# Kernel tuning notes

Measured on AMD Instinct MI355X. Metric: run time of the kernel, lower is better.

The kernel has to match this reference:

```python
import jax, jax.numpy as jnp
import numpy as np

NB, H, C = 6, 4, 192
B, S, L = 2, 64, 256
VOCAB, ED = 24, 64


def setup_inputs() -> dict:
    key = jax.random.key(0)
    ks = iter(jax.random.split(key, 32))
    r = lambda sh: jax.random.normal(next(ks), sh, jnp.float32) * 0.02
    z = lambda sh: jnp.zeros(sh, jnp.float32)
    return {
        'tokens': jax.random.randint(next(ks), (B, S, L), 0, VOCAB, jnp.int32),
        'emb': r((VOCAB, ED)),
        'proj_w': r((C, ED)), 'proj_b': z((C,)),
        'ln_g': jnp.ones((NB, 3, C), jnp.float32), 'ln_b': z((NB, 3, C)),
        'wq': r((NB, 2, C, C)), 'wk': r((NB, 2, C, C)),
        'wv': r((NB, 2, C, C)), 'wo': r((NB, 2, C, C)),
        'bq': z((NB, 2, C)), 'bk': z((NB, 2, C)),
        'bv': z((NB, 2, C)), 'bo': z((NB, 2, C)),
        'ffn_w1': r((NB, 4 * C, C)), 'ffn_b1': z((NB, 4 * C)),
        'ffn_w2': r((NB, C, 4 * C)), 'ffn_b2': z((NB, C)),
        'pw_w': r((C,)), 'pw_b': z(()),
    }


def rotary(x):
    # ESM-style rotary embedding over positions along dim -2, feature dim last.
    d = x.shape[-1]
    inv = 1.0 / (10000.0 ** (jnp.arange(0, d, 2, dtype=jnp.float32) / d))
    t = jnp.arange(x.shape[-2], dtype=jnp.float32)
    f = t[:, None] * inv[None, :]                  # (pos, d/2)
    emb = jnp.concatenate([f, f], axis=-1)         # (pos, d)
    cos, sin = jnp.cos(emb), jnp.sin(emb)
    x1, x2 = jnp.split(x, 2, axis=-1)
    return x * cos + jnp.concatenate([-x2, x1], axis=-1) * sin


def ln_ch(x, g, b, eps=1e-5):
    # LayerNorm over channel axis 1 of (B,C,X,Y) (== transpose->LN->transpose).
    m = x.mean(axis=1, keepdims=True)
    v = jnp.var(x, axis=1, keepdims=True)
    return (x - m) * jax.lax.rsqrt(v + eps) * g[None, :, None, None] + b[None, :, None, None]


def lin_attn(x, wq, wk, wv, wo, bq, bk, bv, bo):
    # ScaledLinearAttention: elu+1 feature map, attends over dim -2 of (B,A,N,C).
    Bm, A, N, Cm = x.shape
    dh = Cm // H
    sh = lambda t: t.reshape(Bm, A, N, H, dh).transpose(0, 1, 3, 2, 4)  # (B,A,H,N,dh)
    q = sh(x @ wq.T + bq)
    k = sh(x @ wk.T + bk)
    v = sh(x @ wv.T + bv)
    q = (jax.nn.elu(q) + 1.0) / jnp.sqrt(jnp.float32(dh))
    k = jax.nn.elu(k) + 1.0
    kv = jnp.einsum('bahnd,bahne->bahde', k, v)
    z = 1.0 / (jnp.einsum('bahnd,bahd->bahn', q, k.sum(axis=-2)) + 1e-6)
    o = jnp.einsum('bahnd,bahde->bahne', q, kv) * z[..., None]
    o = o.transpose(0, 1, 3, 2, 4).reshape(Bm, A, N, Cm)
    return o @ wo.T + bo


def fwd(tokens, emb, proj_w, proj_b, ln_g, ln_b, wq, wk, wv, wo, bq, bk, bv, bo,
        ffn_w1, ffn_b1, ffn_w2, ffn_b2, pw_w, pw_b):
    x = emb[tokens]                    # (B,S,L,ED)
    x = x @ proj_w.T + proj_b          # (B,S,L,C)
    x = rotary(x)                      # rotary over L positions
    out = jnp.transpose(x, (0, 3, 1, 2))  # (B,C,S,L)
    for i in range(NB):
        # row attention (over L)
        h = ln_ch(out, ln_g[i, 0], ln_b[i, 0])
        h = jnp.transpose(h, (0, 2, 3, 1))  # (B,S,L,C)
        h = lin_attn(h, wq[i, 0], wk[i, 0], wv[i, 0], wo[i, 0],
                     bq[i, 0], bk[i, 0], bv[i, 0], bo[i, 0])
        out = out + jnp.transpose(h, (0, 3, 1, 2))
        # col attention (over S)
        h = ln_ch(out, ln_g[i, 1], ln_b[i, 1])
        h = jnp.transpose(h, (0, 3, 2, 1))  # (B,L,S,C)
        h = lin_attn(h, wq[i, 1], wk[i, 1], wv[i, 1], wo[i, 1],
                     bq[i, 1], bk[i, 1], bv[i, 1], bo[i, 1])
        out = out + jnp.transpose(h, (0, 3, 2, 1))
        # 1x1-conv FFN
        h = ln_ch(out, ln_g[i, 2], ln_b[i, 2])
        h = jnp.einsum('bcxy,oc->boxy', h, ffn_w1[i]) + ffn_b1[i][None, :, None, None]
        h = jax.nn.gelu(h, approximate=False)
        h = jnp.einsum('bcxy,oc->boxy', h, ffn_w2[i]) + ffn_b2[i][None, :, None, None]
        out = out + h
    o = jnp.einsum('bcxy,c->bxy', out, pw_w) + pw_b   # pwFNN 1x1 conv to 1 ch
    return jax.nn.sigmoid(jax.nn.softplus(o))


def reference(tokens, emb, proj_w, proj_b, ln_g, ln_b, wq, wk, wv, wo, bq, bk, bv, bo,
              ffn_w1, ffn_b1, ffn_w2, ffn_b2, pw_w, pw_b):
    return fwd(tokens, emb, proj_w, proj_b, ln_g, ln_b, wq, wk, wv, wo, bq, bk, bv, bo,
               ffn_w1, ffn_b1, ffn_w2, ffn_b2, pw_w, pw_b)
```

## Files before the change

kernel.cpp:

```cpp
#include <hip/hip_runtime.h>
#include <hip/hip_bf16.h>
#include <math.h>

#define NBLK 6
#define NH 4
#define CCH 192
#define BB 2
#define SS 64
#define LL 256
#define DH 48
#define NP (BB*SS*LL)
#define BUF ((size_t)NP*CCH)

typedef __attribute__((ext_vector_type(8))) short short8;
typedef __attribute__((ext_vector_type(4))) float float4v;
typedef __attribute__((ext_vector_type(2))) unsigned int uintx2;

__device__ __forceinline__ unsigned short f2b(float f) {
    union { float f; unsigned int u; } v; v.f = f;
    unsigned int r = v.u + 0x7FFF + ((v.u >> 16) & 1);
    return (unsigned short)(r >> 16);
}
__device__ __forceinline__ float b2f(unsigned short u) {
    union { unsigned int u; float f; } v; v.u = ((unsigned int)u) << 16;
    return v.f;
}
__device__ __forceinline__ unsigned int cvt_pk_bf16(float lo, float hi) {
    unsigned int r;
    asm("v_cvt_pk_bf16_f32 %0, %1, %2" : "=v"(r) : "v"(lo), "v"(hi));
    return r;
}
__device__ __forceinline__ void st2u(unsigned short* p0, unsigned short* p1, float a, float b) {
    unsigned int u = cvt_pk_bf16(a, b);
    *p0 = (unsigned short)u;
    *p1 = (unsigned short)(u >> 16);
}
__device__ __forceinline__ void xf_unpack(uintx2 u, float* f) {
    union { unsigned int x; float ff; } t;
    t.x = u[0] << 16;          f[0] = t.ff;
    t.x = u[0] & 0xffff0000u;  f[1] = t.ff;
    t.x = u[1] << 16;          f[2] = t.ff;
    t.x = u[1] & 0xffff0000u;  f[3] = t.ff;
}
__device__ __forceinline__ float gelu_f(float v) {
    float z = v * 0.7071067811865475f;
    float a = fabsf(z);
    float t = __builtin_amdgcn_rcpf(fmaf(0.3275911f, a, 1.0f));
    float p = fmaf(t, 1.061405429f, -1.453152027f);
    p = fmaf(t, p, 1.421413741f);
    p = fmaf(t, p, -0.284496736f);
    p = fmaf(t, p, 0.254829592f);
    p *= t;
    float e = __expf(-a * a);
    float er = fmaf(-p, e, 1.0f);
    er = __builtin_copysignf(er, z);
    return 0.5f * v * (1.0f + er);
}
__device__ __forceinline__ void async_lds16(const void* g, void* l) {
    __builtin_amdgcn_global_load_lds(
        (const __attribute__((address_space(1))) unsigned int*)g,
        (__attribute__((address_space(3))) unsigned int*)l, 16, 0, 0);
}

#define XF(p16, c) (((size_t)(p16) * 192 + (c)) << 4)

template<int N, int K>
__global__ void swz_conv(const float* __restrict__ src, unsigned short* __restrict__ dst, int layers) {
    int s = blockIdx.x * 256 + threadIdx.x;
    if (s >= layers * N * K) return;
    int li = s / (N * K);
    int t = s - li * (N * K);
    constexpr int KC = K / 32;
    int chunk = t >> 9, c = t & 511;
    int g = chunk / KC, sk = chunk - g * KC;
    int lane = c >> 3, ko = c & 7;
    int n = g * 16 + (lane & 15), k = sk * 32 + (lane >> 4) * 8 + ko;
    dst[s] = f2b(src[(size_t)li * N * K + (size_t)n * K + k]);
}
__global__ void wqkv_swz(const float* __restrict__ wq, const float* __restrict__ wk,
                         const float* __restrict__ wv, unsigned short* __restrict__ d) {
    int s = blockIdx.x * 256 + threadIdx.x;
    int wi = s / (576 * 192);
    int t = s - wi * 576 * 192;
    int chunk = t >> 9, c = t & 511;
    int g = chunk / 6, sk = chunk - g * 6;
    int lane = c >> 3, ko = c & 7;
    int n = g * 16 + (lane & 15), k = sk * 32 + (lane >> 4) * 8 + ko;
    int sg = n / 192, row = n - sg * 192;
    const float* src = (sg == 0) ? wq : (sg == 1) ? wk : wv;
    d[s] = f2b(src[(size_t)wi * 192 * 192 + (size_t)row * 192 + k]);
}
__global__ void bqkv_concat(const float* __restrict__ bq, const float* __restrict__ bk,
                            const float* __restrict__ bv, float* __restrict__ d) {
    int idx = blockIdx.x * 256 + threadIdx.x;
    if (idx >= NBLK * 2 * 576) return;
    int wi = idx / 576, n = idx - (idx / 576) * 576;
    int sg = n / 192, row = n - sg * 192;
    const float* src = (sg == 0) ? bq : (sg == 1) ? bk : bv;
    d[idx] = src[wi * CCH + row];
}

__global__ void gather_kernel(const int* __restrict__ tokens, const float* __restrict__ emb,
                              unsigned short* __restrict__ Eg) {
    int idx = blockIdx.x * 256 + threadIdx.x;
    int p = idx >> 6, c = idx & 63;
    Eg[idx] = f2b(emb[tokens[p] * 64 + c]);
}

__global__ __launch_bounds__(256) void rotary_ln_kernel(const float* __restrict__ Xt,
                                                        unsigned short* __restrict__ X,
                                                        unsigned short* __restrict__ Hn,
                                                        const float* __restrict__ g, const float* __restrict__ b) {
    int wave = threadIdx.x >> 6;
    int lane = threadIdx.x & 63;
    int p = blockIdx.x * 4 + wave;
    int l = p & (LL - 1);
    const float* xp = Xt + (size_t)p * CCH;
    float v[3];
    #pragma unroll
    for (int i = 0; i < 3; ++i) {
        int c = lane + i * 64;
        int j = c % 96;
        float inv = expf((float)(2 * j) * (-9.210340371976184f / 192.0f));
        float ang = (float)l * inv;
        float part = (c < 96) ? -xp[c + 96] : xp[c - 96];
        v[i] = xp[c] * cosf(ang) + part * sinf(ang);
    }
    float s = v[0] + v[1] + v[2];
    float qq = v[0] * v[0] + v[1] * v[1] + v[2] * v[2];
    #pragma unroll
    for (int off = 32; off; off >>= 1) {
        s += __shfl_xor(s, off, 64);
        qq += __shfl_xor(qq, off, 64);
    }
    float mean = s * (1.0f / 192.0f);
    float var = qq * (1.0f / 192.0f) - mean * mean;
    float r = rsqrtf(var + 1e-5f);
    unsigned short* hp = Hn + (size_t)p * CCH;
    const int p16 = p >> 4, pr = p & 15;
    #pragma unroll
    for (int i = 0; i < 3; ++i) {
        int c = lane + i * 64;
        X[XF(p16, c) + pr] = f2b(v[i]);
        hp[c] = f2b((v[i] - mean) * r * g[c] + b[c]);
    }
}

template<int MT, int EPI>
__global__ __launch_bounds__(256, (MT == 128) ? 3 : 4)
void mm192(const unsigned short* __restrict__ A, const unsigned short* __restrict__ Wsw,
           const float* __restrict__ bias,
           unsigned short* __restrict__ O0, unsigned short* __restrict__ O1,
           unsigned short* __restrict__ O2,
           float* __restrict__ Of,
           int M, int N, int K) {
    constexpr int NI = MT / 32;
    __shared__ __align__(16) unsigned char lds[(MT == 128) ? 51200 : 28672];
    const int tid = threadIdx.x;
    const int lane = tid & 63;
    const int w = tid >> 6;
    const int wm = w >> 1, wn = w & 1;
    const int m0 = blockIdx.y * MT;
    const int g0 = blockIdx.x * 12;
    const int q = lane >> 4;
    const int q8 = q << 3;
    const int r15 = lane & 15;
    const int KC = K >> 5;

    for (int c = w; c < (MT / 16) * KC; c += 4) {
        int g = c / KC, sk = c - g * KC;
        async_lds16(A + (size_t)(m0 + g * 16 + r15) * K + sk * 32 + q8, lds + c * 1024);
    }

    float4v acc[NI][6];
    #pragma unroll
    for (int i = 0; i < NI; ++i)
        #pragma unroll
        for (int j = 0; j < 6; ++j)
            acc[i][j] = (float4v){0.f, 0.f, 0.f, 0.f};

    __syncthreads();

    for (int sk = 0; sk < KC; ++sk) {
        short8 af[NI], wf[6];
        #pragma unroll
        for (int j = 0; j < 6; ++j)
            wf[j] = *(const short8*)(Wsw + (((size_t)(g0 + wn * 6 + j) * KC + sk) << 9) + lane * 8);
        #pragma unroll
        for (int i = 0; i < NI; ++i)
            af[i] = *(const short8*)(lds + (((wm * NI + i) * KC + sk) << 10) + lane * 16);
        #pragma unroll
        for (int i = 0; i < NI; ++i)
            #pragma unroll
            for (int j = 0; j < 6; ++j)
                acc[i][j] = __builtin_amdgcn_mfma_f32_16x16x32_bf16(af[i], wf[j], acc[i][j], 0, 0, 0);
    }

    const int nb = blockIdx.x * 192 + wn * 96 + r15;
    const int mb = m0 + wm * (MT / 2) + q * 4;

    if (EPI == 0) {
        const int bx = blockIdx.x;
        unsigned short* dst = (bx == 0) ? O0 : (bx == 1) ? O1 : O2;
        #pragma unroll
        for (int j = 0; j < 6; ++j) {
            int n = nb + j * 16;
            int col = wn * 96 + j * 16 + r15;
            float bv = bias[n];
            #pragma unroll
            for (int i = 0; i < NI; ++i) {
                int mrow = wm * (MT / 2) + i * 16 + q * 4;
                #pragma unroll
                for (int r = 0; r < 4; ++r) {
                    float v = acc[i][j][r] + bv;
                    if (bx < 2) v = (v > 0.f) ? v + 1.f : __expf(v);
                    if (bx == 0) v *= 0.14433756729740643f;
                    dst[(size_t)(m0 + mrow + r) * 192 + col] = f2b(v);
                }
            }
        }
    } else {
        #pragma unroll
        for (int j = 0; j < 6; ++j) {
            int n = nb + j * 16;
            float bv = bias[n];
            #pragma unroll
            for (int i = 0; i < NI; ++i) {
                int mrow = mb + i * 16;
                #pragma unroll
                for (int r = 0; r < 4; ++r)
                    Of[(size_t)(mrow + r) * N + n] = acc[i][j][r] + bv;
            }
        }
    }
}


__global__ __launch_bounds__(256, 4)
void wo_qkv(const unsigned short* __restrict__ Ho,
            const unsigned short* __restrict__ WOs, const float* __restrict__ BO,
            unsigned short* __restrict__ Xres,
            const float* __restrict__ lng, const float* __restrict__ lnb,
            const unsigned short* __restrict__ QKVs, const float* __restrict__ bqkv,
            unsigned short* __restrict__ Qb, unsigned short* __restrict__ Kb,
            unsigned short* __restrict__ Vb) {
    __shared__ __align__(16) unsigned char lds[25600];
    unsigned char* Lo = lds;
    float* lsum = (float*)(lds + 12288);
    float* lsq  = lsum + 128;
    unsigned char* Ap = lds + 13312;
    const int tid = threadIdx.x;
    const int lane = tid & 63;
    const int w = tid >> 6;
    const int m0 = blockIdx.x * 32;
    const int q = lane >> 4, q8 = q << 3, r15 = lane & 15;
    const int nb = w * 48 + r15;

    #pragma unroll
    for (int it = 0; it < 3; ++it) {
        int c = it * 4 + w;
        int g = c / 6, sk = c - g * 6;
        async_lds16(Ho + (size_t)(m0 + g * 16 + r15) * 192 + sk * 32 + q8, Lo + c * 1024);
    }
    __syncthreads();

    float4v acc[2][3];
    #pragma unroll
    for (int i = 0; i < 2; ++i)
        #pragma unroll
        for (int j = 0; j < 3; ++j)
            acc[i][j] = (float4v){0.f, 0.f, 0.f, 0.f};
    #pragma unroll
    for (int kk = 0; kk < 6; ++kk) {
        short8 af[2], wf[3];
        #pragma unroll
        for (int j = 0; j < 3; ++j)
            wf[j] = *(const short8*)(WOs + (((size_t)(w * 3 + j) * 6 + kk) << 9) + lane * 8);
        #pragma unroll
        for (int i = 0; i < 2; ++i)
            af[i] = *(const short8*)(Lo + ((i * 6 + kk) << 10) + lane * 16);
        #pragma unroll
        for (int i = 0; i < 2; ++i)
            #pragma unroll
            for (int j = 0; j < 3; ++j)
                acc[i][j] = __builtin_amdgcn_mfma_f32_16x16x32_bf16(af[i], wf[j], acc[i][j], 0, 0, 0);
    }

    #pragma unroll
    for (int j = 0; j < 3; ++j) {
        int n = nb + j * 16;
        float bv = BO[n];
        #pragma unroll
        for (int i = 0; i < 2; ++i) {
            unsigned short* xp = Xres + XF(blockIdx.x * 2 + i, n) + q * 4;
            uintx2 u = *(const uintx2*)xp;
            float f[4]; xf_unpack(u, f);
            #pragma unroll
            for (int r = 0; r < 4; ++r) acc[i][j][r] += bv + f[r];
            uintx2 o;
            o[0] = cvt_pk_bf16(acc[i][j][0], acc[i][j][1]);
            o[1] = cvt_pk_bf16(acc[i][j][2], acc[i][j][3]);
            *(uintx2*)xp = o;
        }
    }
    #pragma unroll
    for (int i = 0; i < 2; ++i)
        #pragma unroll
        for (int r = 0; r < 4; ++r) {
            float s1 = acc[i][0][r] + acc[i][1][r] + acc[i][2][r];
            float s2 = acc[i][0][r] * acc[i][0][r] + acc[i][1][r] * acc[i][1][r] + acc[i][2][r] * acc[i][2][r];
            #pragma unroll
            for (int off = 1; off < 16; off <<= 1) {
                s1 += __shfl_xor(s1, off, 64);
                s2 += __shfl_xor(s2, off, 64);
            }
            if (r15 == 0) {
                int rl = i * 16 + q * 4 + r;
                lsum[rl * 4 + w] = s1;
                lsq[rl * 4 + w] = s2;
            }
        }
    __syncthreads();
    #pragma unroll
    for (int i = 0; i < 2; ++i) {
        float mean[4], rstd[4];
        #pragma unroll
        for (int r = 0; r < 4; ++r) {
            int rl4 = (i * 16 + q * 4 + r) * 4;
            float s  = lsum[rl4] + lsum[rl4 + 1] + lsum[rl4 + 2] + lsum[rl4 + 3];
            float ss = lsq[rl4] + lsq[rl4 + 1] + lsq[rl4 + 2] + lsq[rl4 + 3];
            float m = s * (1.0f / 192.0f);
            mean[r] = m;
            rstd[r] = rsqrtf(ss * (1.0f / 192.0f) - m * m + 1e-5f);
        }
        #pragma unroll
        for (int j = 0; j < 3; ++j) {
            int h = nb + j * 16;
            float gg = lng[h], bb = lnb[h];
            unsigned short* ap = (unsigned short*)Ap + (i * 6 + (h >> 5)) * 512
                               + ((h >> 3) & 3) * 128 + (h & 7) + q * 32;
            float v0 = (acc[i][j][0] - mean[0]) * rstd[0] * gg + bb;
            float v1 = (acc[i][j][1] - mean[1]) * rstd[1] * gg + bb;
            float v2 = (acc[i][j][2] - mean[2]) * rstd[2] * gg + bb;
            float v3 = (acc[i][j][3] - mean[3]) * rstd[3] * gg + bb;
            st2u(ap, ap + 8, v0, v1);
            st2u(ap + 16, ap + 24, v2, v3);
        }
    }
    __syncthreads();

    for (int seg = 0; seg < 3; ++seg) {
        float4v a2[2][3];
        #pragma unroll
        for (int i = 0; i < 2; ++i)
            #pragma unroll
            for (int j = 0; j < 3; ++j)
                a2[i][j] = (float4v){0.f, 0.f, 0.f, 0.f};
        #pragma unroll
        for (int kk = 0; kk < 6; ++kk) {
            short8 af[2], wf[3];
            #pragma unroll
            for (int j = 0; j < 3; ++j)
                wf[j] = *(const short8*)(QKVs + (((size_t)(seg * 12 + w * 3 + j) * 6 + kk) << 9) + lane * 8);
            #pragma unroll
            for (int i = 0; i < 2; ++i)
                af[i] = *(const short8*)(Ap + ((i * 6 + kk) << 10) + lane * 16);
            #pragma unroll
            for (int i = 0; i < 2; ++i)
                #pragma unroll
                for (int j = 0; j < 3; ++j)
                    a2[i][j] = __builtin_amdgcn_mfma_f32_16x16x32_bf16(af[i], wf[j], a2[i][j], 0, 0, 0);
        }
        unsigned short* dst = (seg == 0) ? Qb : (seg == 1) ? Kb : Vb;
        #pragma unroll
        for (int j = 0; j < 3; ++j) {
            int n = nb + j * 16;
            float bv = bqkv[seg * 192 + n];
            #pragma unroll
            for (int i = 0; i < 2; ++i) {
                int mrow = m0 + i * 16 + q * 4;
                #pragma unroll
                for (int r = 0; r < 4; ++r) {
                    float x = a2[i][j][r] + bv;
                    if (seg < 2) x = (x > 0.f) ? x + 1.f : __expf(x);
                    if (seg == 0) x *= 0.14433756729740643f;
                    dst[(size_t)(mrow + r) * 192 + n] = f2b(x);
                }
            }
        }
    }
}

template<bool LASTB>
__global__ __launch_bounds__(256, 4)
void wo_ffn_qkv(const unsigned short* __restrict__ Ho,
                const unsigned short* __restrict__ WOs, const float* __restrict__ BO,
                unsigned short* __restrict__ Xres,
                const float* __restrict__ ln1g, const float* __restrict__ ln1b,
                const unsigned short* __restrict__ W1s, const float* __restrict__ B1,
                const unsigned short* __restrict__ W2s, const float* __restrict__ B2,
                const float* __restrict__ ln2g, const float* __restrict__ ln2b,
                const unsigned short* __restrict__ QKVs, const float* __restrict__ bqkv,
                unsigned short* __restrict__ Qb, unsigned short* __restrict__ Kb,
                unsigned short* __restrict__ Vb) {
    __shared__ __align__(16) unsigned char lds[25600];
    unsigned char* Lo = lds;
    float* lsum = (float*)(lds + 12288);
    float* lsq  = lsum + 128;
    unsigned char* Ap = lds + 13312;
    const int tid = threadIdx.x;
    const int lane = tid & 63;
    const int w = tid >> 6;
    const int m0 = blockIdx.x * 32;
    const int q = lane >> 4, q8 = q << 3, r15 = lane & 15;
    const int nb = w * 48 + r15;

    #pragma unroll
    for (int it = 0; it < 3; ++it) {
        int c = it * 4 + w;
        int g = c / 6, sk = c - g * 6;
        async_lds16(Ho + (size_t)(m0 + g * 16 + r15) * 192 + sk * 32 + q8, Lo + c * 1024);
    }
    __syncthreads();

    float4v xres[2][3];
    #pragma unroll
    for (int i = 0; i < 2; ++i)
        #pragma unroll
        for (int j = 0; j < 3; ++j)
            xres[i][j] = (float4v){0.f, 0.f, 0.f, 0.f};
    #pragma unroll
    for (int kk = 0; kk < 6; ++kk) {
        short8 af[2], wf[3];
        #pragma unroll
        for (int j = 0; j < 3; ++j)
            wf[j] = *(const short8*)(WOs + (((size_t)(w * 3 + j) * 6 + kk) << 9) + lane * 8);
        #pragma unroll
        for (int i = 0; i < 2; ++i)
            af[i] = *(const short8*)(Lo + ((i * 6 + kk) << 10) + lane * 16);
        #pragma unroll
        for (int i = 0; i < 2; ++i)
            #pragma unroll
            for (int j = 0; j < 3; ++j)
                xres[i][j] = __builtin_amdgcn_mfma_f32_16x16x32_bf16(af[i], wf[j], xres[i][j], 0, 0, 0);
    }
    #pragma unroll
    for (int j = 0; j < 3; ++j) {
        int n = nb + j * 16;
        float bv = BO[n];
        #pragma unroll
        for (int i = 0; i < 2; ++i) {
            const unsigned short* xp = Xres + XF(blockIdx.x * 2 + i, n) + q * 4;
            uintx2 u = *(const uintx2*)xp;
            float f[4]; xf_unpack(u, f);
            #pragma unroll
            for (int r = 0; r < 4; ++r) xres[i][j][r] += bv + f[r];
        }
    }
    #pragma unroll
    for (int i = 0; i < 2; ++i)
        #pragma unroll
        for (int r = 0; r < 4; ++r) {
            float s1 = xres[i][0][r] + xres[i][1][r] + xres[i][2][r];
            float s2 = xres[i][0][r] * xres[i][0][r] + xres[i][1][r] * xres[i][1][r] + xres[i][2][r] * xres[i][2][r];
            #pragma unroll
            for (int off = 1; off < 16; off <<= 1) {
                s1 += __shfl_xor(s1, off, 64);
                s2 += __shfl_xor(s2, off, 64);
            }
            if (r15 == 0) {
                int rl = i * 16 + q * 4 + r;
                lsum[rl * 4 + w] = s1;
                lsq[rl * 4 + w] = s2;
            }
        }
    __syncthreads();
    #pragma unroll
    for (int i = 0; i < 2; ++i) {
        float mean[4], rstd[4];
        #pragma unroll
        for (int r = 0; r < 4; ++r) {
            int rl4 = (i * 16 + q * 4 + r) * 4;
            float s  = lsum[rl4] + lsum[rl4 + 1] + lsum[rl4 + 2] + lsum[rl4 + 3];
            float ss = lsq[rl4] + lsq[rl4 + 1] + lsq[rl4 + 2] + lsq[rl4 + 3];
            float m = s * (1.0f / 192.0f);
            mean[r] = m;
            rstd[r] = rsqrtf(ss * (1.0f / 192.0f) - m * m + 1e-5f);
        }
        #pragma unroll
        for (int j = 0; j < 3; ++j) {
            int h = nb + j * 16;
            float gg = ln1g[h], bb = ln1b[h];
            unsigned short* ap = (unsigned short*)Ap + (i * 6 + (h >> 5)) * 512
                               + ((h >> 3) & 3) * 128 + (h & 7) + q * 32;
            float v0 = (xres[i][j][0] - mean[0]) * rstd[0] * gg + bb;
            float v1 = (xres[i][j][1] - mean[1]) * rstd[1] * gg + bb;
            float v2 = (xres[i][j][2] - mean[2]) * rstd[2] * gg + bb;
            float v3 = (xres[i][j][3] - mean[3]) * rstd[3] * gg + bb;
            st2u(ap, ap + 8, v0, v1);
            st2u(ap + 16, ap + 24, v2, v3);
        }
    }
    __syncthreads();

    float4v acc2[2][3];
    #pragma unroll
    for (int i = 0; i < 2; ++i)
        #pragma unroll
        for (int j = 0; j < 3; ++j)
            acc2[i][j] = (float4v){0.f, 0.f, 0.f, 0.f};
    for (int hc = 0; hc < 4; ++hc) {
        float4v acc1[2][3];
        #pragma unroll
        for (int i = 0; i < 2; ++i)
            #pragma unroll
            for (int j = 0; j < 3; ++j)
                acc1[i][j] = (float4v){0.f, 0.f, 0.f, 0.f};
        #pragma unroll
        for (int kk = 0; kk < 6; ++kk) {
            short8 af[2], wf[3];
            #pragma unroll
            for (int j = 0; j < 3; ++j)
                wf[j] = *(const short8*)(W1s + (((size_t)(hc * 12 + w * 3 + j) * 6 + kk) << 9) + lane * 8);
            #pragma unroll
            for (int i = 0; i < 2; ++i)
                af[i] = *(const short8*)(Ap + ((i * 6 + kk) << 10) + lane * 16);
            #pragma unroll
            for (int i = 0; i < 2; ++i)
                #pragma unroll
                for (int j = 0; j < 3; ++j)
                    acc1[i][j] = __builtin_amdgcn_mfma_f32_16x16x32_bf16(af[i], wf[j], acc1[i][j], 0, 0, 0);
        }
        __syncthreads();
        #pragma unroll
        for (int i = 0; i < 2; ++i)
            #pragma unroll
            for (int j = 0; j < 3; ++j) {
                int h = nb + j * 16;
                float bv = B1[hc * 192 + h];
                unsigned short* lp = (unsigned short*)Lo + (i * 6 + (h >> 5)) * 512
                                   + ((h >> 3) & 3) * 128 + (h & 7) + q * 32;
                float v0 = gelu_f(acc1[i][j][0] + bv);
                float v1 = gelu_f(acc1[i][j][1] + bv);
                float v2 = gelu_f(acc1[i][j][2] + bv);
                float v3 = gelu_f(acc1[i][j][3] + bv);
                st2u(lp, lp + 8, v0, v1);
                st2u(lp + 16, lp + 24, v2, v3);
            }
        __syncthreads();
        #pragma unroll
        for (int kk = 0; kk < 6; ++kk) {
            short8 af[2], wf[3];
            #pragma unroll
            for (int j = 0; j < 3; ++j)
                wf[j] = *(const short8*)(W2s + (((size_t)(w * 3 + j) * 24 + hc * 6 + kk) << 9) + lane * 8);
            #pragma unroll
            for (int i = 0; i < 2; ++i)
                af[i] = *(const short8*)(Lo + ((i * 6 + kk) << 10) + lane * 16);
            #pragma unroll
            for (int i = 0; i < 2; ++i)
                #pragma unroll
                for (int j = 0; j < 3; ++j)
                    acc2[i][j] = __builtin_amdgcn_mfma_f32_16x16x32_bf16(af[i], wf[j], acc2[i][j], 0, 0, 0);
        }
    }

    #pragma unroll
    for (int j = 0; j < 3; ++j) {
        int n = nb + j * 16;
        float bv = B2[n];
        #pragma unroll
        for (int i = 0; i < 2; ++i) {
            #pragma unroll
            for (int r = 0; r < 4; ++r)
                xres[i][j][r] += acc2[i][j][r] + bv;
            unsigned short* xp = Xres + XF(blockIdx.x * 2 + i, n) + q * 4;
            uintx2 o;
            o[0] = cvt_pk_bf16(xres[i][j][0], xres[i][j][1]);
            o[1] = cvt_pk_bf16(xres[i][j][2], xres[i][j][3]);
            *(uintx2*)xp = o;
        }
    }
    if (LASTB) return;

    #pragma unroll
    for (int i = 0; i < 2; ++i)
        #pragma unroll
        for (int r = 0; r < 4; ++r) {
            float s1 = xres[i][0][r] + xres[i][1][r] + xres[i][2][r];
            float s2 = xres[i][0][r] * xres[i][0][r] + xres[i][1][r] * xres[i][1][r] + xres[i][2][r] * xres[i][2][r];
            #pragma unroll
            for (int off = 1; off < 16; off <<= 1) {
                s1 += __shfl_xor(s1, off, 64);
                s2 += __shfl_xor(s2, off, 64);
            }
            if (r15 == 0) {
                int rl = i * 16 + q * 4 + r;
                lsum[rl * 4 + w] = s1;
                lsq[rl * 4 + w] = s2;
            }
        }
    __syncthreads();
    #pragma unroll
    for (int i = 0; i < 2; ++i) {
        float mean[4], rstd[4];
        #pragma unroll
        for (int r = 0; r < 4; ++r) {
            int rl4 = (i * 16 + q * 4 + r) * 4;
            float s  = lsum[rl4] + lsum[rl4 + 1] + lsum[rl4 + 2] + lsum[rl4 + 3];
            float ss = lsq[rl4] + lsq[rl4 + 1] + lsq[rl4 + 2] + lsq[rl4 + 3];
            float m = s * (1.0f / 192.0f);
            mean[r] = m;
            rstd[r] = rsqrtf(ss * (1.0f / 192.0f) - m * m + 1e-5f);
        }
        #pragma unroll
        for (int j = 0; j < 3; ++j) {
            int h = nb + j * 16;
            float gg = ln2g[h], bb = ln2b[h];
            unsigned short* ap = (unsigned short*)Ap + (i * 6 + (h >> 5)) * 512
                               + ((h >> 3) & 3) * 128 + (h & 7) + q * 32;
            float v0 = (xres[i][j][0] - mean[0]) * rstd[0] * gg + bb;
            float v1 = (xres[i][j][1] - mean[1]) * rstd[1] * gg + bb;
            float v2 = (xres[i][j][2] - mean[2]) * rstd[2] * gg + bb;
            float v3 = (xres[i][j][3] - mean[3]) * rstd[3] * gg + bb;
            st2u(ap, ap + 8, v0, v1);
            st2u(ap + 16, ap + 24, v2, v3);
        }
    }
    __syncthreads();

    for (int seg = 0; seg < 3; ++seg) {
        float4v a2[2][3];
        #pragma unroll
        for (int i = 0; i < 2; ++i)
            #pragma unroll
            for (int j = 0; j < 3; ++j)
                a2[i][j] = (float4v){0.f, 0.f, 0.f, 0.f};
        #pragma unroll
        for (int kk = 0; kk < 6; ++kk) {
            short8 af[2], wf[3];
            #pragma unroll
            for (int j = 0; j < 3; ++j)
                wf[j] = *(const short8*)(QKVs + (((size_t)(seg * 12 + w * 3 + j) * 6 + kk) << 9) + lane * 8);
            #pragma unroll
            for (int i = 0; i < 2; ++i)
                af[i] = *(const short8*)(Ap + ((i * 6 + kk) << 10) + lane * 16);
            #pragma unroll
            for (int i = 0; i < 2; ++i)
                #pragma unroll
                for (int j = 0; j < 3; ++j)
                    a2[i][j] = __builtin_amdgcn_mfma_f32_16x16x32_bf16(af[i], wf[j], a2[i][j], 0, 0, 0);
        }
        unsigned short* dst = (seg == 0) ? Qb : (seg == 1) ? Kb : Vb;
        #pragma unroll
        for (int j = 0; j < 3; ++j) {
            int n = nb + j * 16;
            float bv = bqkv[seg * 192 + n];
            #pragma unroll
            for (int i = 0; i < 2; ++i) {
                int mrow = m0 + i * 16 + q * 4;
                #pragma unroll
                for (int r = 0; r < 4; ++r) {
                    float x = a2[i][j][r] + bv;
                    if (seg < 2) x = (x > 0.f) ? x + 1.f : __expf(x);
                    if (seg == 0) x *= 0.14433756729740643f;
                    dst[(size_t)(mrow + r) * 192 + n] = f2b(x);
                }
            }
        }
    }
}

template<int N, int MSTR>
__global__ __launch_bounds__(256) void attn_axial(const unsigned short* __restrict__ Qb,
                                                  const unsigned short* __restrict__ Kb,
                                                  const unsigned short* __restrict__ Vb,
                                                  unsigned short* __restrict__ O) {
    __shared__ unsigned short KV[32][400];
    __shared__ unsigned short kvs[4][64][72];
    unsigned char* kvb = (unsigned char*)KV;
    const int tid = threadIdx.x;
    const int lane = tid & 63;
    const int w = tid >> 6;
    const int q = lane >> 4, r15 = lane & 15, q8 = q * 8;
    size_t base;
    if (MSTR == 1) base = (size_t)blockIdx.x * N;
    else           base = (size_t)(blockIdx.x >> 8) * 16384 + (blockIdx.x & 255);

    unsigned int* kz = (unsigned int*)&kvs[w][0][0];
    #pragma unroll
    for (int ii = 0; ii < 36; ++ii) kz[lane + ii * 64] = 0;

    short8 onesf;
    #pragma unroll
    for (int e = 0; e < 8; ++e) onesf[e] = (short)0x3F80;

    float4v kv[3][4];
    #pragma unroll
    for (int i = 0; i < 3; ++i)
        #pragma unroll
        for (int j = 0; j < 4; ++j)
            kv[i][j] = (float4v){0.f, 0.f, 0.f, 0.f};

    for (int ks = 0; ks < N; ks += 32) {
        #pragma unroll
        for (int it = 0; it < 6; ++it) {
            int cc = tid + it * 256;
            int row = cc / 48, c8 = cc - (cc / 48) * 48;
            size_t poff = (base + (size_t)(ks + row) * MSTR) * 192;
            const unsigned short* gp = (c8 < 24) ? (Kb + poff + c8 * 8) : (Vb + poff + (c8 - 24) * 8);
            int ba = (row * 800 + c8 * 16) ^ (((row >> 3) & 3) << 5);
            *(short8*)(kvb + ba) = *(const short8*)gp;
        }
        __syncthreads();
        short8 af[3], bf[3];
        #pragma unroll
        for (int t = 0; t < 3; ++t) {
            #pragma unroll
            for (int j = 0; j < 8; ++j) {
                int row = q8 + j;
                int sw = ((row >> 3) & 3) << 5;
                af[t][j] = *(short*)(kvb + ((row * 800 + (w * 48 + t * 16 + r15) * 2) ^ sw));
                bf[t][j] = *(short*)(kvb + ((row * 800 + 384 + (w * 48 + t * 16 + r15) * 2) ^ sw));
            }
        }
        #pragma unroll
        for (int i = 0; i < 3; ++i) {
            #pragma unroll
            for (int j = 0; j < 3; ++j)
                kv[i][j] = __builtin_amdgcn_mfma_f32_16x16x32_bf16(af[i], bf[j], kv[i][j], 0, 0, 0);
            kv[i][3] = __builtin_amdgcn_mfma_f32_16x16x32_bf16(af[i], onesf, kv[i][3], 0, 0, 0);
        }
        __syncthreads();
    }

    #pragma unroll
    for (int i = 0; i < 3; ++i) {
        #pragma unroll
        for (int j = 0; j < 3; ++j)
            #pragma unroll
            for (int r = 0; r < 4; ++r)
                kvs[w][j * 16 + r15][i * 16 + q * 4 + r] = f2b(kv[i][j][r]);
        if (r15 == 0)
            #pragma unroll
            for (int r = 0; r < 4; ++r)
                kvs[w][48][i * 16 + q * 4 + r] = f2b(kv[i][3][r]);
    }

    short8 bkv[2][4];
    #pragma unroll
    for (int kk = 0; kk < 2; ++kk)
        #pragma unroll
        for (int t = 0; t < 4; ++t)
            bkv[kk][t] = *(const short8*)&kvs[w][t * 16 + r15][kk * 32 + q8];

    for (int mt = 0; mt < N / 16; ++mt) {
        float4v o[4];
        #pragma unroll
        for (int t = 0; t < 4; ++t) o[t] = (float4v){0.f, 0.f, 0.f, 0.f};
        #pragma unroll
        for (int kk = 0; kk < 2; ++kk) {
            const unsigned short* qp = Qb + (base + (size_t)(mt * 16 + r15) * MSTR) * 192
                                       + w * 48 + kk * 32 + q8;
            short8 aq = *(const short8*)qp;
            #pragma unroll
            for (int t = 0; t < 4; ++t)
                o[t] = __builtin_amdgcn_mfma_f32_16x16x32_bf16(aq, bkv[kk][t], o[t], 0, 0, 0);
        }
        #pragma unroll
        for (int r = 0; r < 4; ++r) {
            float den = __shfl(o[3][r], q << 4);
            float z = 1.0f / (den + 1e-6f);
            int n = mt * 16 + q * 4 + r;
            unsigned short* op = O + (base + (size_t)n * MSTR) * 192 + w * 48;
            #pragma unroll
            for (int t = 0; t < 3; ++t)
                op[t * 16 + r15] = f2b(o[t][r] * z);
        }
    }
}

__global__ __launch_bounds__(256) void final_kernel(const unsigned short* __restrict__ X,
                                                    const float* __restrict__ pw_w,
                                                    const float* __restrict__ pw_b, float* __restrict__ out) {
    int wave = threadIdx.x >> 6;
    int lane = threadIdx.x & 63;
    int p = blockIdx.x * 4 + wave;
    const unsigned short* xp = X + XF(p >> 4, 0) + (p & 15);
    float s = b2f(xp[(size_t)lane << 4]) * pw_w[lane]
            + b2f(xp[(size_t)(lane + 64) << 4]) * pw_w[lane + 64]
            + b2f(xp[(size_t)(lane + 128) << 4]) * pw_w[lane + 128];
    #pragma unroll
    for (int off = 32; off; off >>= 1) s += __shfl_xor(s, off, 64);
    if (lane == 0) {
        float o = s + pw_b[0];
        float e = expf(o);
        out[p] = 1.0f - 1.0f / (2.0f + e);
    }
}

extern "C" void kernel_launch(void* const* d_in, const int* in_sizes, int n_in,
                              void* d_out, int out_size, void* d_ws, size_t ws_size,
                              hipStream_t stream) {
    const int*   tokens = (const int*)  d_in[0];
    const float* emb    = (const float*)d_in[1];
    const float* proj_w = (const float*)d_in[2];
    const float* proj_b = (const float*)d_in[3];
    const float* ln_g   = (const float*)d_in[4];
    const float* ln_b   = (const float*)d_in[5];
    const float* wq     = (const float*)d_in[6];
    const float* wk     = (const float*)d_in[7];
    const float* wv     = (const float*)d_in[8];
    const float* wo     = (const float*)d_in[9];
    const float* bq     = (const float*)d_in[10];
    const float* bk     = (const float*)d_in[11];
    const float* bv     = (const float*)d_in[12];
    const float* bo     = (const float*)d_in[13];
    const float* ffn_w1 = (const float*)d_in[14];
    const float* ffn_b1 = (const float*)d_in[15];
    const float* ffn_w2 = (const float*)d_in[16];
    const float* ffn_b2 = (const float*)d_in[17];
    const float* pw_w   = (const float*)d_in[18];
    const float* pw_b   = (const float*)d_in[19];

    unsigned short* X    = (unsigned short*)d_ws;
    unsigned short* Ho   = X + BUF;
    unsigned short* Qb   = Ho + BUF;
    unsigned short* Kb   = Qb + BUF;
    unsigned short* Vb   = Kb + BUF;
    unsigned short* Eg   = Vb + BUF;
    unsigned short* wqkvb = Eg + (size_t)NP * 64;
    const int QKVSZ = NBLK * 2 * 576 * CCH;
    const int WSZ   = NBLK * 2 * CCH * CCH;
    const int FSZ   = NBLK * 768 * CCH;
    unsigned short* wob = wqkvb + QKVSZ;
    unsigned short* w1b = wob + WSZ;
    unsigned short* w2b = w1b + FSZ;
    unsigned short* pjb = w2b + FSZ;
    float* bqkvb = (float*)(pjb + 12288 + 32);
    float* Xt = (float*)Qb;

    wqkv_swz<<<QKVSZ / 256, 256, 0, stream>>>(wq, wk, wv, wqkvb);
    bqkv_concat<<<27, 256, 0, stream>>>(bq, bk, bv, bqkvb);
    swz_conv<192, 192><<<(WSZ + 255) / 256, 256, 0, stream>>>(wo, wob, NBLK * 2);
    swz_conv<768, 192><<<(FSZ + 255) / 256, 256, 0, stream>>>(ffn_w1, w1b, NBLK);
    swz_conv<192, 768><<<(FSZ + 255) / 256, 256, 0, stream>>>(ffn_w2, w2b, NBLK);
    swz_conv<192, 64><<<48, 256, 0, stream>>>(proj_w, pjb, 1);

    gather_kernel<<<NP * 64 / 256, 256, 0, stream>>>(tokens, emb, Eg);
    mm192<64, 1><<<dim3(1, NP / 64), 256, 0, stream>>>(Eg, pjb, proj_b,
                                                       nullptr, nullptr, nullptr, Xt, NP, CCH, 64);
    rotary_ln_kernel<<<NP / 4, 256, 0, stream>>>(Xt, X, Ho, ln_g, ln_b);
    mm192<128, 0><<<dim3(3, NP / 128), 256, 0, stream>>>(Ho, wqkvb, bqkvb,
                                                         Qb, Kb, Vb, nullptr, NP, 576, CCH);

    for (int i = 0; i < NBLK; ++i) {
        size_t wi0 = (size_t)(i * 2), wi1 = wi0 + 1;
        attn_axial<LL, 1><<<BB * SS, 256, 0, stream>>>(Qb, Kb, Vb, Ho);
        wo_qkv<<<NP / 32, 256, 0, stream>>>(Ho, wob + wi0 * CCH * CCH, bo + wi0 * CCH, X,
                                            ln_g + (size_t)(i * 3 + 1) * CCH, ln_b + (size_t)(i * 3 + 1) * CCH,
                                            wqkvb + wi1 * 576 * CCH, bqkvb + wi1 * 576, Qb, Kb, Vb);
        attn_axial<SS, LL><<<BB * LL, 256, 0, stream>>>(Qb, Kb, Vb, Ho);
        if (i < NBLK - 1) {
            size_t wn0 = (size_t)((i + 1) * 2);
            wo_ffn_qkv<false><<<NP / 32, 256, 0, stream>>>(
                Ho, wob + wi1 * CCH * CCH, bo + wi1 * CCH, X,
                ln_g + (size_t)(i * 3 + 2) * CCH, ln_b + (size_t)(i * 3 + 2) * CCH,
                w1b + (size_t)i * 768 * CCH, ffn_b1 + (size_t)i * 768,
                w2b + (size_t)i * CCH * 768, ffn_b2 + (size_t)i * CCH,
                ln_g + (size_t)((i + 1) * 3) * CCH, ln_b + (size_t)((i + 1) * 3) * CCH,
                wqkvb + wn0 * 576 * CCH, bqkvb + wn0 * 576, Qb, Kb, Vb);
        } else {
            wo_ffn_qkv<true><<<NP / 32, 256, 0, stream>>>(
                Ho, wob + wi1 * CCH * CCH, bo + wi1 * CCH, X,
                ln_g + (size_t)(i * 3 + 2) * CCH, ln_b + (size_t)(i * 3 + 2) * CCH,
                w1b + (size_t)i * 768 * CCH, ffn_b1 + (size_t)i * 768,
                w2b + (size_t)i * CCH * 768, ffn_b2 + (size_t)i * CCH,
                nullptr, nullptr, nullptr, nullptr, nullptr, nullptr, nullptr);
        }
    }
    final_kernel<<<NP / 4, 256, 0, stream>>>(X, pw_w, pw_b, (float*)d_out);
}
```

Baseline: 878.4 us.

## Store K/V channel-major for row attention and add dedicated MFMA row-attention kernel

The QKV projection epilogues that feed row attention now write K and V transposed (channel-major per (b,s) row, packed bf16x4 stores), while Q keeps its layout. A new attn_row kernel stages the transposed K/V tiles in LDS and computes the KV outer product and the K-sum (via a ones vector) with MFMA, then applies the result to Q. The aim is coalesced K/V reads and fewer scattered 2-byte stores for the row-attention pass. The new layout must match every consumer, and the column-attention path is left unchanged even though it reads the same buffers.

New measurement: 918.1 us. 1.05x slower.

```diff
diff --git a/kernel.cpp b/kernel.cpp
--- a/kernel.cpp
+++ b/kernel.cpp
@@ -201,21 +201,48 @@
 
     if (EPI == 0) {
         const int bx = blockIdx.x;
-        unsigned short* dst = (bx == 0) ? O0 : (bx == 1) ? O1 : O2;
-        #pragma unroll
-        for (int j = 0; j < 6; ++j) {
-            int n = nb + j * 16;
-            int col = wn * 96 + j * 16 + r15;
-            float bv = bias[n];
-            #pragma unroll
-            for (int i = 0; i < NI; ++i) {
-                int mrow = wm * (MT / 2) + i * 16 + q * 4;
+        if (bx == 0) {
+            #pragma unroll
+            for (int j = 0; j < 6; ++j) {
+                int n = nb + j * 16;
+                int col = wn * 96 + j * 16 + r15;
+                float bv = bias[n];
                 #pragma unroll
-                for (int r = 0; r < 4; ++r) {
-                    float v = acc[i][j][r] + bv;
-                    if (bx < 2) v = (v > 0.f) ? v + 1.f : __expf(v);
-                    if (bx == 0) v *= 0.14433756729740643f;
-                    dst[(size_t)(m0 + mrow + r) * 192 + col] = f2b(v);
+                for (int i = 0; i < NI; ++i) {
+                    int mrow = wm * (MT / 2) + i * 16 + q * 4;
+                    #pragma unroll
+                    for (int r = 0; r < 4; ++r) {
+                        float v = acc[i][j][r] + bv;
+                        v = (v > 0.f) ? v + 1.f : __expf(v);
+                        v *= 0.14433756729740643f;
+                        O0[(size_t)(m0 + mrow + r) * 192 + col] = f2b(v);
+                    }
+                }
+            }
+        } else {
+            unsigned short* dst = (bx == 1) ? O1 : O2;
+            const int bs_ = m0 >> 8;
+            const int l0 = m0 & 255;
+            #pragma unroll
+            for (int j = 0; j < 6; ++j) {
+                int n = nb + j * 16;
+                int col = wn * 96 + j * 16 + r15;
+                float bv = bias[n];
+                #pragma unroll
+                for (int i = 0; i < NI; ++i) {
+                    int mrow = wm * (MT / 2) + i * 16 + q * 4;
+                    float x[4];
+                    #pragma unroll
+                    for (int r = 0; r < 4; ++r) {
+                        float v = acc[i][j][r] + bv;
+                        if (bx == 1) v = (v > 0.f) ? v + 1.f : __expf(v);
+                        x[r] = v;
+                    }
+                    size_t base = (size_t)bs_ * 49152 + (size_t)col * 256 + l0 + mrow;
+                    uintx2 o;
+                    o[0] = cvt_pk_bf16(x[0], x[1]);
+                    o[1] = cvt_pk_bf16(x[2], x[3]);
+                    *(uintx2*)(dst + base) = o;
                 }
             }
         }
@@ -349,6 +376,7 @@
     }
     __syncthreads();
 
+    #pragma unroll
     for (int seg = 0; seg < 3; ++seg) {
         float4v a2[2][3];
         #pragma unroll
@@ -629,6 +657,9 @@
     }
     __syncthreads();
 
+    const int bs_ = m0 >> 8;
+    const int l0 = m0 & 255;
+    #pragma unroll
     for (int seg = 0; seg < 3; ++seg) {
         float4v a2[2][3];
         #pragma unroll
@@ -651,22 +682,156 @@
                 for (int j = 0; j < 3; ++j)
                     a2[i][j] = __builtin_amdgcn_mfma_f32_16x16x32_bf16(af[i], wf[j], a2[i][j], 0, 0, 0);
         }
-        unsigned short* dst = (seg == 0) ? Qb : (seg == 1) ? Kb : Vb;
-        #pragma unroll
-        for (int j = 0; j < 3; ++j) {
-            int n = nb + j * 16;
-            float bv = bqkv[seg * 192 + n];
-            #pragma unroll
-            for (int i = 0; i < 2; ++i) {
-                int mrow = m0 + i * 16 + q * 4;
+        if (seg == 0) {
+            #pragma unroll
+            for (int j = 0; j < 3; ++j) {
+                int n = nb + j * 16;
+                float bv = bqkv[n];
                 #pragma unroll
-                for (int r = 0; r < 4; ++r) {
-                    float x = a2[i][j][r] + bv;
-                    if (seg < 2) x = (x > 0.f) ? x + 1.f : __expf(x);
-                    if (seg == 0) x *= 0.14433756729740643f;
-                    dst[(size_t)(mrow + r) * 192 + n] = f2b(x);
+                for (int i = 0; i < 2; ++i) {
+                    int mrow = m0 + i * 16 + q * 4;
+                    #pragma unroll
+                    for (int r = 0; r < 4; ++r) {
+                        float x = a2[i][j][r] + bv;
+                        x = (x > 0.f) ? x + 1.f : __expf(x);
+                        x *= 0.14433756729740643f;
+                        Qb[(size_t)(mrow + r) * 192 + n] = f2b(x);
+                    }
                 }
             }
+        } else {
+            unsigned short* dst = (seg == 1) ? Kb : Vb;
+            #pragma unroll
+            for (int j = 0; j < 3; ++j) {
+                int n = nb + j * 16;
+                float bv = bqkv[seg * 192 + n];
+                #pragma unroll
+                for (int i = 0; i < 2; ++i) {
+                    float x[4];
+                    #pragma unroll
+                    for (int r = 0; r < 4; ++r) {
+                        float v = a2[i][j][r] + bv;
+                        if (seg == 1) v = (v > 0.f) ? v + 1.f : __expf(v);
+                        x[r] = v;
+                    }
+                    size_t base = (size_t)bs_ * 49152 + (size_t)n * 256 + l0 + i * 16 + q * 4;
+                    uintx2 o;
+                    o[0] = cvt_pk_bf16(x[0], x[1]);
+                    o[1] = cvt_pk_bf16(x[2], x[3]);
+                    *(uintx2*)(dst + base) = o;
+                }
+            }
+        }
+    }
+}
+
+__global__ __launch_bounds__(256) void attn_row(const unsigned short* __restrict__ Qb,
+                                                const unsigned short* __restrict__ Kt,
+                                                const unsigned short* __restrict__ Vt,
+                                                unsigned short* __restrict__ O) {
+    __shared__ __align__(16) unsigned char lds[36864];
+    unsigned short* ldsK = (unsigned short*)lds;
+    unsigned short* ldsV = (unsigned short*)(lds + 15360);
+    auto kvs = (unsigned short (*)[64][72])lds;
+    const int tid = threadIdx.x;
+    const int lane = tid & 63;
+    const int w = tid >> 6;
+    const int q = lane >> 4, r15 = lane & 15, q8 = q * 8;
+    const size_t base = (size_t)blockIdx.x * 256;
+    const size_t kb = (size_t)blockIdx.x * 49152;
+
+    short8 onesf;
+    #pragma unroll
+    for (int e = 0; e < 8; ++e) onesf[e] = (short)0x3F80;
+
+    float4v kv[3][4];
+    #pragma unroll
+    for (int i = 0; i < 3; ++i)
+        #pragma unroll
+        for (int j = 0; j < 4; ++j)
+            kv[i][j] = (float4v){0.f, 0.f, 0.f, 0.f};
+
+    for (int ks = 0; ks < 256; ks += 32) {
+        short8 kreg[3], vreg[3];
+        #pragma unroll
+        for (int it = 0; it < 3; ++it) {
+            int idx = it * 256 + tid;
+            int c = idx >> 2, part = idx & 3;
+            kreg[it] = *(const short8*)(Kt + kb + c * 256 + ks + part * 8);
+            vreg[it] = *(const short8*)(Vt + kb + c * 256 + ks + part * 8);
+        }
+        __syncthreads();
+        #pragma unroll
+        for (int it = 0; it < 3; ++it) {
+            int idx = it * 256 + tid;
+            int c = idx >> 2, part = idx & 3;
+            *(short8*)(ldsK + c * 40 + part * 8) = kreg[it];
+            *(short8*)(ldsV + c * 40 + part * 8) = vreg[it];
+        }
+        __syncthreads();
+        short8 af[3], bf[3];
+        #pragma unroll
+        for (int t = 0; t < 3; ++t) {
+            int c = w * 48 + t * 16 + r15;
+            af[t] = *(const short8*)(ldsK + c * 40 + q8);
+            bf[t] = *(const short8*)(ldsV + c * 40 + q8);
+        }
+        #pragma unroll
+        for (int i = 0; i < 3; ++i) {
+            #pragma unroll
+            for (int j = 0; j < 3; ++j)
+                kv[i][j] = __builtin_amdgcn_mfma_f32_16x16x32_bf16(af[i], bf[j], kv[i][j], 0, 0, 0);
+            kv[i][3] = __builtin_amdgcn_mfma_f32_16x16x32_bf16(af[i], onesf, kv[i][3], 0, 0, 0);
+        }
+    }
+    __syncthreads();
+
+    unsigned int* kz = (unsigned int*)&kvs[w][0][0];
+    #pragma unroll
+    for (int ii = 0; ii < 36; ++ii) kz[lane + ii * 64] = 0;
+
+    #pragma unroll
+    for (int i = 0; i < 3; ++i) {
+        #pragma unroll
+        for (int j = 0; j < 3; ++j)
+            #pragma unroll
+            for (int r = 0; r < 4; ++r)
+                kvs[w][j * 16 + r15][i * 16 + q * 4 + r] = f2b(kv[i][j][r]);
+        if (r15 == 0)
+            #pragma unroll
+            for (int r = 0; r < 4; ++r)
+                kvs[w][48][i * 16 + q * 4 + r] = f2b(kv[i][3][r]);
+    }
+
+    short8 bkv[2][4];
+    #pragma unroll
+    for (int kk = 0; kk < 2; ++kk)
+        #pragma unroll
+        for (int t = 0; t < 4; ++t)
+            bkv[kk][t] = *(const short8*)&kvs[w][t * 16 + r15][kk * 32 + q8];
+
+    for (int mt = 0; mt < 16; ++mt) {
+        float4v o[4];
+        #pragma unroll
+        for (int t = 0; t < 4; ++t) o[t] = (float4v){0.f, 0.f, 0.f, 0.f};
+        #pragma unroll
+        for (int kk = 0; kk < 2; ++kk) {
+            const unsigned short* qp = Qb + (base + (size_t)(mt * 16 + r15)) * 192
+                                       + w * 48 + kk * 32 + q8;
+            short8 aq = *(const short8*)qp;
+            #pragma unroll
+            for (int t = 0; t < 4; ++t)
+                o[t] = __builtin_amdgcn_mfma_f32_16x16x32_bf16(aq, bkv[kk][t], o[t], 0, 0, 0);
+        }
+        #pragma unroll
+        for (int r = 0; r < 4; ++r) {
+            float den = __shfl(o[3][r], q << 4);
+            float z = 1.0f / (den + 1e-6f);
+            int n = mt * 16 + q * 4 + r;
+            unsigned short* op = O + (base + (size_t)n) * 192 + w * 48;
+            #pragma unroll
+            for (int t = 0; t < 3; ++t)
+                op[t * 16 + r15] = f2b(o[t][r] * z);
         }
     }
 }
@@ -856,7 +1021,7 @@
 
     for (int i = 0; i < NBLK; ++i) {
         size_t wi0 = (size_t)(i * 2), wi1 = wi0 + 1;
-        attn_axial<LL, 1><<<BB * SS, 256, 0, stream>>>(Qb, Kb, Vb, Ho);
+        attn_row<<<BB * SS, 256, 0, stream>>>(Qb, Kb, Vb, Ho);
         wo_qkv<<<NP / 32, 256, 0, stream>>>(Ho, wob + wi0 * CCH * CCH, bo + wi0 * CCH, X,
                                             ln_g + (size_t)(i * 3 + 1) * CCH, ln_b + (size_t)(i * 3 + 1) * CCH,
                                             wqkvb + wi1 * 576 * CCH, bqkvb + wi1 * 576, Qb, Kb, Vb);
```
